# Optimization experiments

Hardware: AMD Instinct MI355X
Metric: run time of the kernel (lower is better)

Reference implementation:

```python
import jax, jax.numpy as jnp
import numpy as np

N_NODES = 50000
N_EDGES = 800000
IN_FEATS = 256
OUT_FEATS = 32
NUM_HEADS = 8
NUM_ETYPES = 5


def setup_inputs() -> dict:
    key = jax.random.key(0)
    k1, k2, k3, k4, k5, k6 = jax.random.split(key, 6)
    feat = jax.random.normal(k1, (N_NODES, IN_FEATS), dtype=jnp.float32)
    # xavier_normal-ish scale for fc weight [H*D, in]
    fc_w = jax.random.normal(k2, (NUM_HEADS * OUT_FEATS, IN_FEATS), dtype=jnp.float32) * 0.088
    edge_emb = jax.random.normal(k3, (NUM_ETYPES, NUM_HEADS), dtype=jnp.float32)
    e_feat = jax.random.randint(k4, (N_EDGES,), 0, NUM_ETYPES)
    src = jax.random.randint(k5, (N_EDGES,), 0, N_NODES)
    dst = jax.random.randint(k6, (N_EDGES,), 0, N_NODES)
    return {"feat": feat, "fc_w": fc_w, "edge_emb": edge_emb,
            "e_feat": e_feat, "src": src, "dst": dst}


def reference(feat, fc_w, edge_emb, e_feat, src, dst):
    N = feat.shape[0]
    H, D = NUM_HEADS, OUT_FEATS
    # fc: [N, in] @ [in, H*D] -> [N, H, D]
    feat_src = (feat @ fc_w.T).reshape(N, H, D)
    # per-edge, per-head logits from edge-type embedding: [E, H]
    e = edge_emb[e_feat]
    # edge_softmax: softmax over incoming edges of each dst node, per head
    m = jax.ops.segment_max(e, dst, num_segments=N)          # [N, H]
    ex = jnp.exp(e - m[dst])                                  # [E, H]
    denom = jax.ops.segment_sum(ex, dst, num_segments=N)     # [N, H]
    attn = ex / denom[dst]                                    # [E, H]
    # attn_sum: sum of attention weights arriving at each dst (== 1 w/o dropout)
    attn_sum = jax.ops.segment_sum(attn, dst, num_segments=N)  # [N, H]
    # weighted aggregation: sum_e attn_e * feat_src[src_e]
    msg = feat_src[src] * attn[:, :, None]                    # [E, H, D]
    agg = jax.ops.segment_sum(msg, dst, num_segments=N)      # [N, H, D]
    rst = agg / (attn_sum[:, :, None] + 1e-12)
    return rst, attn
```

## Files before the change

kernel.cpp:

```cpp
#include <hip/hip_runtime.h>

typedef unsigned short u16;
typedef unsigned int u32;
typedef __attribute__((ext_vector_type(8))) short bf16x8;
typedef __attribute__((ext_vector_type(4))) float f32x4;

#define NND 50000
#define NE 800000
#define NH 8
#define ND 32
#define NTY 5

__device__ inline u16 f2bf(float x){
  u32 u = __float_as_uint(x);
  return (u16)((u + 0x7FFFu + ((u >> 16) & 1u)) >> 16);
}
__device__ inline float bf2f(u16 h){ return __uint_as_float(((u32)h) << 16); }

#define TM 128
#define LDK 72

__global__ __launch_bounds__(256) void gemm_k(const float* __restrict__ A,
                                              const float* __restrict__ W,
                                              u16* __restrict__ C, int M){
  __shared__ u16 As[TM * LDK];
  __shared__ u16 Bs[TM * LDK];
  const int tid  = threadIdx.x;
  const int m0   = blockIdx.x * TM;
  const int n0   = blockIdx.y * TM;
  const int lane = tid & 63;
  const int wid  = tid >> 6;
  const int wm   = (wid >> 1) * 64, wn = (wid & 1) * 64;
  const int ml   = lane & 15, quad = lane >> 4;

  f32x4 acc[4][4] = {};

  const int sr = tid >> 4;
  const int sc = (tid & 15) * 4;
  const float* aB = A + (size_t)m0 * 256 + sc;
  const float* bB = W + (size_t)n0 * 256 + sc;
  u16* asl = As + sr * LDK + sc;
  u16* bsl = Bs + sr * LDK + sc;

  for (int k0 = 0; k0 < 256; k0 += 64){
    #pragma unroll
    for (int j = 0; j < 8; j++){
      int row = sr + j * 16;
      bool aval = (m0 + row) < M;
      float4 fa = aval ? *(const float4*)(aB + (size_t)row * 256 + k0) : make_float4(0,0,0,0);
      float4 fb = *(const float4*)(bB + (size_t)row * 256 + k0);
      *(ushort4*)(asl + j * 16 * LDK) = make_ushort4(f2bf(fa.x), f2bf(fa.y), f2bf(fa.z), f2bf(fa.w));
      *(ushort4*)(bsl + j * 16 * LDK) = make_ushort4(f2bf(fb.x), f2bf(fb.y), f2bf(fb.z), f2bf(fb.w));
    }
    __syncthreads();
    #pragma unroll
    for (int kk = 0; kk < 64; kk += 32){
      bf16x8 af[4], bfr[4];
      #pragma unroll
      for (int t = 0; t < 4; t++)
        af[t] = *(const bf16x8*)(As + (wm + t * 16 + ml) * LDK + kk + quad * 8);
      #pragma unroll
      for (int t = 0; t < 4; t++)
        bfr[t] = *(const bf16x8*)(Bs + (wn + t * 16 + ml) * LDK + kk + quad * 8);
      #pragma unroll
      for (int i = 0; i < 4; i++)
        #pragma unroll
        for (int j = 0; j < 4; j++)
          acc[i][j] = __builtin_amdgcn_mfma_f32_16x16x32_bf16(af[i], bfr[j], acc[i][j], 0, 0, 0);
    }
    __syncthreads();
  }
  #pragma unroll
  for (int i = 0; i < 4; i++){
    #pragma unroll
    for (int rr = 0; rr < 4; rr++){
      int row = m0 + wm + i * 16 + quad * 4 + rr;
      if (row < M){
        u16* crow = C + (size_t)row * 256 + n0 + wn;
        #pragma unroll
        for (int j = 0; j < 4; j++)
          crow[j * 16 + ml] = f2bf(acc[i][j][rr]);
      }
    }
  }
}

__global__ __launch_bounds__(256) void count_k(const int* __restrict__ dst,
                                               const int* __restrict__ ef,
                                               int* __restrict__ cnt){
  int e = blockIdx.x * 256 + threadIdx.x;
  if (e < NE) atomicAdd(&cnt[dst[e] * NTY + ef[e]], 1);
}

__global__ __launch_bounds__(256) void scan1_k(const int* __restrict__ cnt,
                                               int* __restrict__ offs,
                                               int* __restrict__ bsum){
  __shared__ int lds[256];
  int b = blockIdx.x, tid = threadIdx.x;
  int base = b * 1024 + tid * 4;
  int d[4]; int tsum = 0;
  #pragma unroll
  for (int j = 0; j < 4; j++){
    int node = base + j; int v = 0;
    if (node < NND){
      #pragma unroll
      for (int t = 0; t < NTY; t++) v += cnt[node * NTY + t];
    }
    d[j] = tsum; tsum += v;
  }
  lds[tid] = tsum; __syncthreads();
  for (int off = 1; off < 256; off <<= 1){
    int v = (tid >= off) ? lds[tid - off] : 0;
    __syncthreads();
    lds[tid] += v;
    __syncthreads();
  }
  int incl = lds[tid];
  int excl = incl - tsum;
  #pragma unroll
  for (int j = 0; j < 4; j++)
    if (base + j < NND) offs[base + j] = excl + d[j];
  if (tid == 255) bsum[b] = incl;
}

__global__ __launch_bounds__(64) void scan2_k(const int* __restrict__ bsum,
                                              int* __restrict__ bbase, int nb){
  __shared__ int l[64];
  int tid = threadIdx.x;
  int v = (tid < nb) ? bsum[tid] : 0;
  l[tid] = v; __syncthreads();
  for (int off = 1; off < 64; off <<= 1){
    int u = (tid >= off) ? l[tid - off] : 0;
    __syncthreads();
    l[tid] += u;
    __syncthreads();
  }
  bbase[tid] = l[tid] - v;
}

__global__ __launch_bounds__(256) void scan3_k(int* __restrict__ offs,
                                               int* __restrict__ cursor,
                                               const int* __restrict__ bbase){
  int i = blockIdx.x * 256 + threadIdx.x;
  if (i < NND){
    int v = offs[i] + bbase[i >> 10];
    offs[i] = v; cursor[i] = v;
  }
}

__global__ __launch_bounds__(256) void denom_k(const int* __restrict__ cnt,
                                               const float* __restrict__ emb,
                                               float* __restrict__ rdenom){
  __shared__ float wl[40];
  int tid = threadIdx.x;
  if (tid < 40){
    int t = tid >> 3, h = tid & 7;
    float m = emb[h];
    for (int tt = 1; tt < NTY; ++tt) m = fmaxf(m, emb[tt * 8 + h]);
    wl[tid] = expf(emb[t * 8 + h] - m);
  }
  __syncthreads();
  int n = blockIdx.x * 256 + tid;
  if (n >= NND) return;
  int c[NTY];
  #pragma unroll
  for (int t = 0; t < NTY; t++) c[t] = cnt[n * NTY + t];
  #pragma unroll
  for (int h = 0; h < NH; h++){
    float dsum = 0.f;
    #pragma unroll
    for (int t = 0; t < NTY; t++) dsum += (float)c[t] * wl[t * 8 + h];
    rdenom[n * 8 + h] = (dsum > 0.f) ? (1.f / dsum) : 0.f;
  }
}

__global__ __launch_bounds__(256) void scatter_attn_k(const int* __restrict__ dst,
                                                      const int* __restrict__ src,
                                                      const int* __restrict__ ef,
                                                      int* __restrict__ cursor,
                                                      int* __restrict__ csr,
                                                      const float* __restrict__ emb,
                                                      const float* __restrict__ rdenom,
                                                      float* __restrict__ attn){
  __shared__ float wl[40];
  int tid = threadIdx.x;
  if (tid < 40){
    int t = tid >> 3, h = tid & 7;
    float m = emb[h];
    for (int tt = 1; tt < NTY; ++tt) m = fmaxf(m, emb[tt * 8 + h]);
    wl[tid] = expf(emb[t * 8 + h] - m);
  }
  __syncthreads();
  int e = blockIdx.x * 256 + tid;
  if (e >= NE) return;
  int d = dst[e], t = ef[e];
  int pos = atomicAdd(&cursor[d], 1);
  csr[pos] = src[e] | (t << 16);
  float4 r0 = *(const float4*)(rdenom + (size_t)d * 8);
  float4 r1 = *(const float4*)(rdenom + (size_t)d * 8 + 4);
  const float* wr = wl + t * 8;
  float4 o0 = make_float4(wr[0] * r0.x, wr[1] * r0.y, wr[2] * r0.z, wr[3] * r0.w);
  float4 o1 = make_float4(wr[4] * r1.x, wr[5] * r1.y, wr[6] * r1.z, wr[7] * r1.w);
  *(float4*)(attn + (size_t)e * 8) = o0;
  *(float4*)(attn + (size_t)e * 8 + 4) = o1;
}

__device__ inline void acc8(uint4 v, float wt, float* a){
  a[0] += wt * __uint_as_float(v.x << 16);
  a[1] += wt * __uint_as_float(v.x & 0xFFFF0000u);
  a[2] += wt * __uint_as_float(v.y << 16);
  a[3] += wt * __uint_as_float(v.y & 0xFFFF0000u);
  a[4] += wt * __uint_as_float(v.z << 16);
  a[5] += wt * __uint_as_float(v.z & 0xFFFF0000u);
  a[6] += wt * __uint_as_float(v.w << 16);
  a[7] += wt * __uint_as_float(v.w & 0xFFFF0000u);
}

__global__ __launch_bounds__(256) void agg_k(const u16* __restrict__ fsrc,
                                             const int* __restrict__ csr,
                                             const int* __restrict__ offs,
                                             const int* __restrict__ cursor,
                                             const float* __restrict__ rdenom,
                                             const float* __restrict__ emb,
                                             float* __restrict__ rst){
  __shared__ float wl[40];
  int tid = threadIdx.x;
  if (tid < 40){
    int t = tid >> 3, h = tid & 7;
    float m = emb[h];
    for (int tt = 1; tt < NTY; ++tt) m = fmaxf(m, emb[tt * 8 + h]);
    wl[tid] = expf(emb[t * 8 + h] - m);
  }
  __syncthreads();
  int node = blockIdx.x * 8 + (tid >> 5);
  int sl = tid & 31;
  int c = sl * 8;
  int h = sl >> 2;
  float rd = rdenom[(size_t)node * 8 + h];
  int s = offs[node], e = cursor[node];
  float a[8] = {0,0,0,0,0,0,0,0};
  float ss = 0.f;
  int i = s;
  for (; i + 1 < e; i += 2){
    int pc0 = csr[i], pc1 = csr[i + 1];
    uint4 v0 = *(const uint4*)(fsrc + (size_t)(pc0 & 0xFFFF) * 256 + c);
    uint4 v1 = *(const uint4*)(fsrc + (size_t)(pc1 & 0xFFFF) * 256 + c);
    float w0 = wl[(((u32)pc0) >> 16) * 8 + h] * rd;
    float w1 = wl[(((u32)pc1) >> 16) * 8 + h] * rd;
    acc8(v0, w0, a);
    acc8(v1, w1, a);
    ss += w0 + w1;
  }
  if (i < e){
    int pc0 = csr[i];
    uint4 v0 = *(const uint4*)(fsrc + (size_t)(pc0 & 0xFFFF) * 256 + c);
    float w0 = wl[(((u32)pc0) >> 16) * 8 + h] * rd;
    acc8(v0, w0, a);
    ss += w0;
  }
  float inv = 1.0f / (ss + 1e-12f);
  float* orow = rst + (size_t)node * 256 + c;
  *(float4*)(orow)     = make_float4(a[0] * inv, a[1] * inv, a[2] * inv, a[3] * inv);
  *(float4*)(orow + 4) = make_float4(a[4] * inv, a[5] * inv, a[6] * inv, a[7] * inv);
}

extern "C" void kernel_launch(void* const* d_in, const int* in_sizes, int n_in,
                              void* d_out, int out_size, void* d_ws, size_t ws_size,
                              hipStream_t stream) {
  const float* feat = (const float*)d_in[0];
  const float* fcw  = (const float*)d_in[1];
  const float* emb  = (const float*)d_in[2];
  const int*   ef   = (const int*)d_in[3];
  const int*   src  = (const int*)d_in[4];
  const int*   dst  = (const int*)d_in[5];

  float* rst  = (float*)d_out;
  float* attn = (float*)d_out + (size_t)NND * NH * ND;

  char* ws = (char*)d_ws;
  size_t o = 0;
  u16* fsrc    = (u16*)(ws + o);   o += (size_t)NND * 256 * 2;
  int* csr     = (int*)(ws + o);   o += (size_t)NE * 4;
  int* offs    = (int*)(ws + o);   o += 200064;
  int* cursor  = (int*)(ws + o);   o += 200064;
  int* cnt     = (int*)(ws + o);   o += (size_t)NND * NTY * 4;
  float* rden  = (float*)(ws + o); o += (size_t)NND * NH * 4;
  int* bsum    = (int*)(ws + o);   o += 256;
  int* bbase   = (int*)(ws + o);   o += 256;

  hipMemsetAsync(cnt, 0, (size_t)NND * NTY * 4, stream);

  gemm_k<<<dim3((NND + TM - 1) / TM, 2), 256, 0, stream>>>(feat, fcw, fsrc, NND);
  count_k<<<(NE + 255) / 256, 256, 0, stream>>>(dst, ef, cnt);
  scan1_k<<<(NND + 1023) / 1024, 256, 0, stream>>>(cnt, offs, bsum);
  scan2_k<<<1, 64, 0, stream>>>(bsum, bbase, (NND + 1023) / 1024);
  scan3_k<<<(NND + 255) / 256, 256, 0, stream>>>(offs, cursor, bbase);
  denom_k<<<(NND + 255) / 256, 256, 0, stream>>>(cnt, emb, rden);
  scatter_attn_k<<<(NE + 255) / 256, 256, 0, stream>>>(dst, src, ef, cursor, csr, emb, rden, attn);
  agg_k<<<NND / 8, 256, 0, stream>>>(fsrc, csr, offs, cursor, rden, emb, rst);
}
```

Measured before the change: 300.9 us.

## Restructure GEMM tiling and CSR build with recorded edge positions

```diff
diff --git a/kernel.cpp b/kernel.cpp
--- a/kernel.cpp
+++ b/kernel.cpp
@@ -15,58 +15,67 @@
   u32 u = __float_as_uint(x);
   return (u16)((u + 0x7FFFu + ((u >> 16) & 1u)) >> 16);
 }
-__device__ inline float bf2f(u16 h){ return __uint_as_float(((u32)h) << 16); }
-
-#define TM 128
-#define LDK 72
-
-__global__ __launch_bounds__(256) void gemm_k(const float* __restrict__ A,
-                                              const float* __restrict__ W,
-                                              u16* __restrict__ C, int M){
-  __shared__ u16 As[TM * LDK];
-  __shared__ u16 Bs[TM * LDK];
+
+__global__ __launch_bounds__(512, 4) void gemm_k(const float* __restrict__ A,
+                                                 const float* __restrict__ W,
+                                                 u16* __restrict__ C, int M){
+  __shared__ float As[128 * 64];
+  __shared__ u16  Ws[256 * 64];
   const int tid  = threadIdx.x;
-  const int m0   = blockIdx.x * TM;
-  const int n0   = blockIdx.y * TM;
-  const int lane = tid & 63;
-  const int wid  = tid >> 6;
-  const int wm   = (wid >> 1) * 64, wn = (wid & 1) * 64;
-  const int ml   = lane & 15, quad = lane >> 4;
+  const int m0   = blockIdx.x * 128;
+  const int lane = tid & 63, wid = tid >> 6;
+  const int wm = (wid >> 2) * 64, wn = (wid & 3) * 64;
+  const int ml = lane & 15, quad = lane >> 4;
 
   f32x4 acc[4][4] = {};
 
-  const int sr = tid >> 4;
-  const int sc = (tid & 15) * 4;
-  const float* aB = A + (size_t)m0 * 256 + sc;
-  const float* bB = W + (size_t)n0 * 256 + sc;
-  u16* asl = As + sr * LDK + sc;
-  u16* bsl = Bs + sr * LDK + sc;
+  const int ra = tid >> 2, ca = (tid & 3) * 4;
+  int rag = m0 + ra; if (rag >= M) rag = M - 1;
+  const float* aRow = A + (size_t)rag * 256;
+  const int rw = tid >> 1, hw = tid & 1;
+  const float* wRow = W + (size_t)rw * 256;
 
   for (int k0 = 0; k0 < 256; k0 += 64){
     #pragma unroll
-    for (int j = 0; j < 8; j++){
-      int row = sr + j * 16;
-      bool aval = (m0 + row) < M;
-      float4 fa = aval ? *(const float4*)(aB + (size_t)row * 256 + k0) : make_float4(0,0,0,0);
-      float4 fb = *(const float4*)(bB + (size_t)row * 256 + k0);
-      *(ushort4*)(asl + j * 16 * LDK) = make_ushort4(f2bf(fa.x), f2bf(fa.y), f2bf(fa.z), f2bf(fa.w));
-      *(ushort4*)(bsl + j * 16 * LDK) = make_ushort4(f2bf(fb.x), f2bf(fb.y), f2bf(fb.z), f2bf(fb.w));
+    for (int q = 0; q < 4; q++){
+      float4 v = *(const float4*)(aRow + k0 + (ca + q) * 4);
+      *(float4*)(As + ra * 64 + (((ca + q) ^ (ra & 15)) * 4)) = v;
     }
+    #pragma unroll
+    for (int q = 0; q < 4; q++){
+      int ck = hw * 4 + q;
+      float4 u0 = *(const float4*)(wRow + k0 + ck * 8);
+      float4 u1 = *(const float4*)(wRow + k0 + ck * 8 + 4);
+      ushort4 h0 = make_ushort4(f2bf(u0.x), f2bf(u0.y), f2bf(u0.z), f2bf(u0.w));
+      ushort4 h1 = make_ushort4(f2bf(u1.x), f2bf(u1.y), f2bf(u1.z), f2bf(u1.w));
+      int cp = ck ^ (rw & 7);
+      *(ushort4*)(Ws + rw * 64 + cp * 8) = h0;
+      *(ushort4*)(Ws + rw * 64 + cp * 8 + 4) = h1;
+    }
     __syncthreads();
     #pragma unroll
     for (int kk = 0; kk < 64; kk += 32){
-      bf16x8 af[4], bfr[4];
+      bf16x8 af[4], wf[4];
       #pragma unroll
-      for (int t = 0; t < 4; t++)
-        af[t] = *(const bf16x8*)(As + (wm + t * 16 + ml) * LDK + kk + quad * 8);
+      for (int t = 0; t < 4; t++){
+        int r = wm + t * 16 + ml;
+        int c0 = (kk >> 2) + quad * 2;
+        float4 x0 = *(const float4*)(As + r * 64 + (((c0    ) ^ (r & 15)) * 4));
+        float4 x1 = *(const float4*)(As + r * 64 + (((c0 + 1) ^ (r & 15)) * 4));
+        af[t] = (bf16x8){ (short)f2bf(x0.x), (short)f2bf(x0.y), (short)f2bf(x0.z), (short)f2bf(x0.w),
+                          (short)f2bf(x1.x), (short)f2bf(x1.y), (short)f2bf(x1.z), (short)f2bf(x1.w) };
+      }
       #pragma unroll
-      for (int t = 0; t < 4; t++)
-        bfr[t] = *(const bf16x8*)(Bs + (wn + t * 16 + ml) * LDK + kk + quad * 8);
+      for (int t = 0; t < 4; t++){
+        int n = wn + t * 16 + ml;
+        int c = (kk >> 3) + quad;
+        wf[t] = *(const bf16x8*)(Ws + n * 64 + ((c ^ (n & 7)) * 8));
+      }
       #pragma unroll
       for (int i = 0; i < 4; i++)
         #pragma unroll
         for (int j = 0; j < 4; j++)
-          acc[i][j] = __builtin_amdgcn_mfma_f32_16x16x32_bf16(af[i], bfr[j], acc[i][j], 0, 0, 0);
+          acc[i][j] = __builtin_amdgcn_mfma_f32_16x16x32_bf16(af[i], wf[j], acc[i][j], 0, 0, 0);
     }
     __syncthreads();
   }
@@ -76,7 +85,7 @@
     for (int rr = 0; rr < 4; rr++){
       int row = m0 + wm + i * 16 + quad * 4 + rr;
       if (row < M){
-        u16* crow = C + (size_t)row * 256 + n0 + wn;
+        u16* crow = C + (size_t)row * 256 + wn;
         #pragma unroll
         for (int j = 0; j < 4; j++)
           crow[j * 16 + ml] = f2bf(acc[i][j][rr]);
@@ -86,13 +95,13 @@
 }
 
 __global__ __launch_bounds__(256) void count_k(const int* __restrict__ dst,
-                                               const int* __restrict__ ef,
-                                               int* __restrict__ cnt){
+                                               int* __restrict__ deg,
+                                               int* __restrict__ epos){
   int e = blockIdx.x * 256 + threadIdx.x;
-  if (e < NE) atomicAdd(&cnt[dst[e] * NTY + ef[e]], 1);
-}
-
-__global__ __launch_bounds__(256) void scan1_k(const int* __restrict__ cnt,
+  if (e < NE) epos[e] = atomicAdd(&deg[dst[e]], 1);
+}
+
+__global__ __launch_bounds__(256) void scan1_k(const int* __restrict__ deg,
                                                int* __restrict__ offs,
                                                int* __restrict__ bsum){
   __shared__ int lds[256];
@@ -101,11 +110,8 @@
   int d[4]; int tsum = 0;
   #pragma unroll
   for (int j = 0; j < 4; j++){
-    int node = base + j; int v = 0;
-    if (node < NND){
-      #pragma unroll
-      for (int t = 0; t < NTY; t++) v += cnt[node * NTY + t];
-    }
+    int node = base + j;
+    int v = (node < NND) ? deg[node] : 0;
     d[j] = tsum; tsum += v;
   }
   lds[tid] = tsum; __syncthreads();
@@ -115,12 +121,11 @@
     lds[tid] += v;
     __syncthreads();
   }
-  int incl = lds[tid];
-  int excl = incl - tsum;
+  int excl = lds[tid] - tsum;
   #pragma unroll
   for (int j = 0; j < 4; j++)
     if (base + j < NND) offs[base + j] = excl + d[j];
-  if (tid == 255) bsum[b] = incl;
+  if (tid == 255) bsum[b] = lds[tid];
 }
 
 __global__ __launch_bounds__(64) void scan2_k(const int* __restrict__ bsum,
@@ -138,19 +143,26 @@
   bbase[tid] = l[tid] - v;
 }
 
-__global__ __launch_bounds__(256) void scan3_k(int* __restrict__ offs,
-                                               int* __restrict__ cursor,
-                                               const int* __restrict__ bbase){
-  int i = blockIdx.x * 256 + threadIdx.x;
-  if (i < NND){
-    int v = offs[i] + bbase[i >> 10];
-    offs[i] = v; cursor[i] = v;
-  }
-}
-
-__global__ __launch_bounds__(256) void denom_k(const int* __restrict__ cnt,
-                                               const float* __restrict__ emb,
-                                               float* __restrict__ rdenom){
+__global__ __launch_bounds__(256) void scatter_k(const int* __restrict__ dst,
+                                                 const int* __restrict__ src,
+                                                 const int* __restrict__ ef,
+                                                 const int* __restrict__ epos,
+                                                 const int* __restrict__ offs,
+                                                 const int* __restrict__ bbase,
+                                                 int* __restrict__ csr){
+  int e = blockIdx.x * 256 + threadIdx.x;
+  if (e >= NE) return;
+  int d = dst[e];
+  int pos = offs[d] + bbase[d >> 10] + epos[e];
+  csr[pos] = src[e] | (ef[e] << 16);
+}
+
+__global__ __launch_bounds__(256) void nden_k(const int* __restrict__ csr,
+                                              const int* __restrict__ offs,
+                                              const int* __restrict__ bbase,
+                                              const int* __restrict__ deg,
+                                              const float* __restrict__ emb,
+                                              float* __restrict__ rd){
   __shared__ float wl[40];
   int tid = threadIdx.x;
   if (tid < 40){
@@ -162,26 +174,24 @@
   __syncthreads();
   int n = blockIdx.x * 256 + tid;
   if (n >= NND) return;
-  int c[NTY];
+  int s = offs[n] + bbase[n >> 10];
+  int dcnt = deg[n];
+  float sum[8] = {0,0,0,0,0,0,0,0};
+  for (int i = 0; i < dcnt; i++){
+    int t = ((u32)csr[s + i]) >> 16;
+    #pragma unroll
+    for (int h = 0; h < 8; h++) sum[h] += wl[t * 8 + h];
+  }
   #pragma unroll
-  for (int t = 0; t < NTY; t++) c[t] = cnt[n * NTY + t];
-  #pragma unroll
-  for (int h = 0; h < NH; h++){
-    float dsum = 0.f;
-    #pragma unroll
-    for (int t = 0; t < NTY; t++) dsum += (float)c[t] * wl[t * 8 + h];
-    rdenom[n * 8 + h] = (dsum > 0.f) ? (1.f / dsum) : 0.f;
-  }
-}
-
-__global__ __launch_bounds__(256) void scatter_attn_k(const int* __restrict__ dst,
-                                                      const int* __restrict__ src,
-                                                      const int* __restrict__ ef,
-                                                      int* __restrict__ cursor,
-                                                      int* __restrict__ csr,
-                                                      const float* __restrict__ emb,
-                                                      const float* __restrict__ rdenom,
-                                                      float* __restrict__ attn){
+  for (int h = 0; h < 8; h++)
+    rd[(size_t)n * 8 + h] = (sum[h] > 0.f) ? (1.f / sum[h]) : 0.f;
+}
+
+__global__ __launch_bounds__(256) void attn_k(const int* __restrict__ dst,
+                                              const int* __restrict__ ef,
+                                              const float* __restrict__ rd,
+                                              const float* __restrict__ emb,
+                                              float* __restrict__ attn){
   __shared__ float wl[40];
   int tid = threadIdx.x;
   if (tid < 40){
@@ -194,15 +204,11 @@
   int e = blockIdx.x * 256 + tid;
   if (e >= NE) return;
   int d = dst[e], t = ef[e];
-  int pos = atomicAdd(&cursor[d], 1);
-  csr[pos] = src[e] | (t << 16);
-  float4 r0 = *(const float4*)(rdenom + (size_t)d * 8);
-  float4 r1 = *(const float4*)(rdenom + (size_t)d * 8 + 4);
+  float4 r0 = *(const float4*)(rd + (size_t)d * 8);
+  float4 r1 = *(const float4*)(rd + (size_t)d * 8 + 4);
   const float* wr = wl + t * 8;
-  float4 o0 = make_float4(wr[0] * r0.x, wr[1] * r0.y, wr[2] * r0.z, wr[3] * r0.w);
-  float4 o1 = make_float4(wr[4] * r1.x, wr[5] * r1.y, wr[6] * r1.z, wr[7] * r1.w);
-  *(float4*)(attn + (size_t)e * 8) = o0;
-  *(float4*)(attn + (size_t)e * 8 + 4) = o1;
+  *(float4*)(attn + (size_t)e * 8)     = make_float4(wr[0]*r0.x, wr[1]*r0.y, wr[2]*r0.z, wr[3]*r0.w);
+  *(float4*)(attn + (size_t)e * 8 + 4) = make_float4(wr[4]*r1.x, wr[5]*r1.y, wr[6]*r1.z, wr[7]*r1.w);
 }
 
 __device__ inline void acc8(uint4 v, float wt, float* a){
@@ -219,8 +225,8 @@
 __global__ __launch_bounds__(256) void agg_k(const u16* __restrict__ fsrc,
                                              const int* __restrict__ csr,
                                              const int* __restrict__ offs,
-                                             const int* __restrict__ cursor,
-                                             const float* __restrict__ rdenom,
+                                             const int* __restrict__ bbase,
+                                             const int* __restrict__ deg,
                                              const float* __restrict__ emb,
                                              float* __restrict__ rst){
   __shared__ float wl[40];
@@ -236,32 +242,35 @@
   int sl = tid & 31;
   int c = sl * 8;
   int h = sl >> 2;
-  float rd = rdenom[(size_t)node * 8 + h];
-  int s = offs[node], e = cursor[node];
+  int s = offs[node] + bbase[node >> 10];
+  int e = s + deg[node];
   float a[8] = {0,0,0,0,0,0,0,0};
   float ss = 0.f;
   int i = s;
-  for (; i + 1 < e; i += 2){
-    int pc0 = csr[i], pc1 = csr[i + 1];
-    uint4 v0 = *(const uint4*)(fsrc + (size_t)(pc0 & 0xFFFF) * 256 + c);
-    uint4 v1 = *(const uint4*)(fsrc + (size_t)(pc1 & 0xFFFF) * 256 + c);
-    float w0 = wl[(((u32)pc0) >> 16) * 8 + h] * rd;
-    float w1 = wl[(((u32)pc1) >> 16) * 8 + h] * rd;
-    acc8(v0, w0, a);
-    acc8(v1, w1, a);
-    ss += w0 + w1;
-  }
-  if (i < e){
-    int pc0 = csr[i];
-    uint4 v0 = *(const uint4*)(fsrc + (size_t)(pc0 & 0xFFFF) * 256 + c);
-    float w0 = wl[(((u32)pc0) >> 16) * 8 + h] * rd;
+  for (; i + 3 < e; i += 4){
+    int p0 = csr[i], p1 = csr[i+1], p2 = csr[i+2], p3 = csr[i+3];
+    uint4 v0 = *(const uint4*)(fsrc + (size_t)(p0 & 0xFFFF) * 256 + c);
+    uint4 v1 = *(const uint4*)(fsrc + (size_t)(p1 & 0xFFFF) * 256 + c);
+    uint4 v2 = *(const uint4*)(fsrc + (size_t)(p2 & 0xFFFF) * 256 + c);
+    uint4 v3 = *(const uint4*)(fsrc + (size_t)(p3 & 0xFFFF) * 256 + c);
+    float w0 = wl[(((u32)p0) >> 16) * 8 + h];
+    float w1 = wl[(((u32)p1) >> 16) * 8 + h];
+    float w2 = wl[(((u32)p2) >> 16) * 8 + h];
+    float w3 = wl[(((u32)p3) >> 16) * 8 + h];
+    acc8(v0, w0, a); acc8(v1, w1, a); acc8(v2, w2, a); acc8(v3, w3, a);
+    ss += (w0 + w1) + (w2 + w3);
+  }
+  for (; i < e; i++){
+    int p0 = csr[i];
+    uint4 v0 = *(const uint4*)(fsrc + (size_t)(p0 & 0xFFFF) * 256 + c);
+    float w0 = wl[(((u32)p0) >> 16) * 8 + h];
     acc8(v0, w0, a);
     ss += w0;
   }
   float inv = 1.0f / (ss + 1e-12f);
   float* orow = rst + (size_t)node * 256 + c;
-  *(float4*)(orow)     = make_float4(a[0] * inv, a[1] * inv, a[2] * inv, a[3] * inv);
-  *(float4*)(orow + 4) = make_float4(a[4] * inv, a[5] * inv, a[6] * inv, a[7] * inv);
+  *(float4*)(orow)     = make_float4(a[0]*inv, a[1]*inv, a[2]*inv, a[3]*inv);
+  *(float4*)(orow + 4) = make_float4(a[4]*inv, a[5]*inv, a[6]*inv, a[7]*inv);
 }
 
 extern "C" void kernel_launch(void* const* d_in, const int* in_sizes, int n_in,
@@ -281,21 +290,21 @@
   size_t o = 0;
   u16* fsrc    = (u16*)(ws + o);   o += (size_t)NND * 256 * 2;
   int* csr     = (int*)(ws + o);   o += (size_t)NE * 4;
+  int* epos    = (int*)(ws + o);   o += (size_t)NE * 4;
   int* offs    = (int*)(ws + o);   o += 200064;
-  int* cursor  = (int*)(ws + o);   o += 200064;
-  int* cnt     = (int*)(ws + o);   o += (size_t)NND * NTY * 4;
-  float* rden  = (float*)(ws + o); o += (size_t)NND * NH * 4;
+  int* deg     = (int*)(ws + o);   o += 200064;
+  float* rd    = (float*)(ws + o); o += (size_t)NND * NH * 4;
   int* bsum    = (int*)(ws + o);   o += 256;
   int* bbase   = (int*)(ws + o);   o += 256;
 
-  hipMemsetAsync(cnt, 0, (size_t)NND * NTY * 4, stream);
-
-  gemm_k<<<dim3((NND + TM - 1) / TM, 2), 256, 0, stream>>>(feat, fcw, fsrc, NND);
-  count_k<<<(NE + 255) / 256, 256, 0, stream>>>(dst, ef, cnt);
-  scan1_k<<<(NND + 1023) / 1024, 256, 0, stream>>>(cnt, offs, bsum);
+  hipMemsetAsync(deg, 0, (size_t)NND * 4, stream);
+
+  gemm_k<<<391, 512, 0, stream>>>(feat, fcw, fsrc, NND);
+  count_k<<<(NE + 255) / 256, 256, 0, stream>>>(dst, deg, epos);
+  scan1_k<<<(NND + 1023) / 1024, 256, 0, stream>>>(deg, offs, bsum);
   scan2_k<<<1, 64, 0, stream>>>(bsum, bbase, (NND + 1023) / 1024);
-  scan3_k<<<(NND + 255) / 256, 256, 0, stream>>>(offs, cursor, bbase);
-  denom_k<<<(NND + 255) / 256, 256, 0, stream>>>(cnt, emb, rden);
-  scatter_attn_k<<<(NE + 255) / 256, 256, 0, stream>>>(dst, src, ef, cursor, csr, emb, rden, attn);
-  agg_k<<<NND / 8, 256, 0, stream>>>(fsrc, csr, offs, cursor, rden, emb, rst);
-}
+  scatter_k<<<(NE + 255) / 256, 256, 0, stream>>>(dst, src, ef, epos, offs, bbase, csr);
+  nden_k<<<(NND + 255) / 256, 256, 0, stream>>>(csr, offs, bbase, deg, emb, rd);
+  attn_k<<<(NE + 255) / 256, 256, 0, stream>>>(dst, ef, rd, emb, attn);
+  agg_k<<<NND / 8, 256, 0, stream>>>(fsrc, csr, offs, bbase, deg, emb, rst);
+}
```

After: 285.2 us. 1.06x faster.
